# Kernel optimization log

Measured on AMD Instinct MI355X. Metric: run time of the kernel, lower is better.

Reference implementation:

```python
import jax, jax.numpy as jnp
import numpy as np

D_MODEL = 768
NUM_HEADS = 12
D_K = D_MODEL // NUM_HEADS
D_FF = 2048
LN_EPS = 1e-3  # Keras LayerNormalization default
B, S = 4, 2048


def layer_norm(x, gamma, beta):
    mu = jnp.mean(x, axis=-1, keepdims=True)
    var = jnp.var(x, axis=-1, keepdims=True)
    return (x - mu) * jax.lax.rsqrt(var + LN_EPS) * gamma + beta


def setup_inputs() -> dict:
    key = jax.random.key(0)
    ks = jax.random.split(key, 16)
    sd = 0.02
    inp = {
        "x": jax.random.normal(ks[0], (B, S, D_MODEL), dtype=jnp.float32),
        "src_mask": jnp.zeros((B, 1, 1, S), dtype=jnp.float32),
        "Wq": jax.random.normal(ks[1], (D_MODEL, D_MODEL), jnp.float32) * sd,
        "bq": jnp.zeros((D_MODEL,), jnp.float32),
        "Wk": jax.random.normal(ks[2], (D_MODEL, D_MODEL), jnp.float32) * sd,
        "bk": jnp.zeros((D_MODEL,), jnp.float32),
        "Wv": jax.random.normal(ks[3], (D_MODEL, D_MODEL), jnp.float32) * sd,
        "bv": jnp.zeros((D_MODEL,), jnp.float32),
        "Wo": jax.random.normal(ks[4], (D_MODEL, D_MODEL), jnp.float32) * sd,
        "bo": jnp.zeros((D_MODEL,), jnp.float32),
        "W1": jax.random.normal(ks[5], (D_MODEL, D_FF), jnp.float32) * sd,
        "b1": jnp.zeros((D_FF,), jnp.float32),
        "W2": jax.random.normal(ks[6], (D_FF, D_MODEL), jnp.float32) * sd,
        "b2": jnp.zeros((D_MODEL,), jnp.float32),
        "gamma1": jnp.ones((D_MODEL,), jnp.float32),
        "beta1": jnp.zeros((D_MODEL,), jnp.float32),
        "gamma2": jnp.ones((D_MODEL,), jnp.float32),
        "beta2": jnp.zeros((D_MODEL,), jnp.float32),
    }
    return inp


def encoder_layer(x, src_mask, Wq, bq, Wk, bk, Wv, bv, Wo, bo, W1, b1, W2, b2,
                  gamma1, beta1, gamma2, beta2):
    b, s, _ = x.shape
    def heads(t):  # [B,S,D] -> [B,H,S,Dk]
        return t.reshape(b, s, NUM_HEADS, D_K).transpose(0, 2, 1, 3)
    Q = heads(x @ Wq + bq)
    K = heads(x @ Wk + bk)
    V = heads(x @ Wv + bv)
    scores = jnp.einsum("bhqd,bhkd->bhqk", Q, K) / jnp.sqrt(jnp.float32(D_K))
    scores = scores + src_mask * (-1e9)
    probs = jax.nn.softmax(scores, axis=-1)
    attn = jnp.einsum("bhqk,bhkd->bhqd", probs, V)
    attn = attn.transpose(0, 2, 1, 3).reshape(b, s, D_MODEL)
    attn_out = attn @ Wo + bo
    # dropout is identity at inference
    x1 = layer_norm(x + attn_out, gamma1, beta1)
    ff = jax.nn.relu(x1 @ W1 + b1) @ W2 + b2
    return layer_norm(x1 + ff, gamma2, beta2)


def reference(x, src_mask, Wq, bq, Wk, bk, Wv, bv, Wo, bo, W1, b1, W2, b2,
              gamma1, beta1, gamma2, beta2):
    return encoder_layer(x, src_mask, Wq, bq, Wk, bk, Wv, bv, Wo, bo,
                         W1, b1, W2, b2, gamma1, beta1, gamma2, beta2)
```

## Files before the change

kernel.cpp:

```cpp
#include <hip/hip_runtime.h>


typedef unsigned short u16;
typedef __bf16 bf16x8 __attribute__((ext_vector_type(8)));
typedef __bf16 bf16x4 __attribute__((ext_vector_type(4)));
typedef unsigned short u16x8 __attribute__((ext_vector_type(8)));
typedef float f32x4 __attribute__((ext_vector_type(4)));

#define D_MODEL 768
#define D_FF    2048
#define NH      12
#define DK      64
#define S_LEN   2048
#define M_TOK   8192

#define QSCALE   0.18033688011112042f
#define MSCALE  -1.4426950408889634e9f

__device__ __forceinline__ float bf2f(u16 v) {
    union { unsigned u; float f; } c; c.u = ((unsigned)v) << 16; return c.f;
}
__device__ __forceinline__ void st_bf(u16* p, float v) { *(__bf16*)p = (__bf16)v; }

__device__ __forceinline__ void gload_lds16(const void* g, void* l) {
    __builtin_amdgcn_global_load_lds(
        (const __attribute__((address_space(1))) void*)g,
        (__attribute__((address_space(3))) void*)l, 16, 0, 0);
}

__global__ __launch_bounds__(256)
void prep_k(const float* __restrict__ x, const float* __restrict__ Wq,
            const float* __restrict__ Wk, const float* __restrict__ Wv,
            const float* __restrict__ Wo, const float* __restrict__ W1,
            const float* __restrict__ W2, u16* __restrict__ xb,
            u16* __restrict__ WqkvT, u16* __restrict__ WoT,
            u16* __restrict__ W1T, u16* __restrict__ W2T) {
    __shared__ float t[32][33];
    const int id = blockIdx.x, tid = threadIdx.x;
    if (id >= 5376) {
        const int i = ((id - 5376) * 256 + tid) * 4;
        const float4 v = *(const float4*)(x + i);
        __bf16 o[4] = {(__bf16)v.x, (__bf16)v.y, (__bf16)v.z, (__bf16)v.w};
        *(bf16x4*)(xb + i) = *(bf16x4*)o;
        return;
    }
    const float* in; u16* out; int R, C, bx, by;
    if (id < 2304) {
        const int z = id / 576, r = id % 576;
        in = z == 0 ? Wq : (z == 1 ? Wk : (z == 2 ? Wv : Wo));
        out = z == 3 ? WoT : WqkvT + z * 768 * 768;
        R = 768; C = 768; bx = (r % 24) * 32; by = (r / 24) * 32;
    } else if (id < 3840) {
        const int r = id - 2304;
        in = W1; out = W1T; R = 768; C = 2048;
        bx = (r % 64) * 32; by = (r / 64) * 32;
    } else {
        const int r = id - 3840;
        in = W2; out = W2T; R = 2048; C = 768;
        bx = (r % 24) * 32; by = (r / 24) * 32;
    }
    const int tx = tid & 31, ty = tid >> 5;
#pragma unroll
    for (int i = 0; i < 32; i += 8)
        t[ty + i][tx] = in[(size_t)(by + ty + i) * C + bx + tx];
    __syncthreads();
#pragma unroll
    for (int i = 0; i < 32; i += 8)
        st_bf(&out[(size_t)(bx + ty + i) * R + by + tx], t[tx][ty + i]);
}

__global__ __launch_bounds__(256, 2)
void qkv_gemm_k(const u16* __restrict__ A, const u16* __restrict__ Bt,
                const float* __restrict__ bq, const float* __restrict__ bk,
                const float* __restrict__ bv, u16* __restrict__ Qb,
                u16* __restrict__ Kb, u16* __restrict__ Vt) {
    __shared__ __align__(16) u16 As[2][128 * 32];
    __shared__ __align__(16) u16 Bs[2][128 * 32];
    const int tid = threadIdx.x;
    const int lane = tid & 63, w = tid >> 6;
    const int r16 = lane & 15, qd = lane >> 4;
    const int m0 = blockIdx.x * 128, n0 = blockIdx.y * 128;
    const int wm = (w & 1) << 6, wn = (w >> 1) << 6;
    const int K = D_MODEL;

    f32x4 acc[4][4] = {};

    const u16* aP[2]; const u16* bP[2]; int f8[2];
#pragma unroll
    for (int it = 0; it < 2; ++it) {
        const int f = it * 256 + tid;
        const int row = f >> 2, kc = (f & 3) << 3;
        aP[it] = A  + (size_t)(m0 + row) * K + kc;
        bP[it] = Bt + (size_t)(n0 + row) * K + kc;
        f8[it] = f * 8;
    }

    for (int k0 = 0; k0 < K; k0 += 64) {
#pragma unroll
        for (int p = 0; p < 2; ++p)
#pragma unroll
            for (int it = 0; it < 2; ++it) {
                gload_lds16(aP[it] + k0 + p * 32, &As[p][f8[it]]);
                gload_lds16(bP[it] + k0 + p * 32, &Bs[p][f8[it]]);
            }
        __syncthreads();
#pragma unroll
        for (int p = 0; p < 2; ++p) {
            bf16x8 af[4], bfr[4];
#pragma unroll
            for (int i = 0; i < 4; ++i) {
                af[i]  = *(const bf16x8*)&As[p][(wm + i * 16 + r16) * 32 + qd * 8];
                bfr[i] = *(const bf16x8*)&Bs[p][(wn + i * 16 + r16) * 32 + qd * 8];
            }
#pragma unroll
            for (int i = 0; i < 4; ++i)
#pragma unroll
                for (int j = 0; j < 4; ++j)
                    acc[i][j] = __builtin_amdgcn_mfma_f32_16x16x32_bf16(af[i], bfr[j], acc[i][j], 0, 0, 0);
        }
        __syncthreads();
    }

    const int sel = n0 < 768 ? 0 : (n0 < 1536 ? 1 : 2);
    const float* bias = sel == 0 ? bq : (sel == 1 ? bk : bv);
    const float scale = sel == 0 ? QSCALE : 1.0f;
    const int nbase = n0 - sel * 768;

#pragma unroll
    for (int j = 0; j < 4; ++j) {
        const int ncol = nbase + wn + j * 16 + r16;
        const float bvv = bias[ncol];
#pragma unroll
        for (int i = 0; i < 4; ++i) {
            if (sel == 2) {
                const int h = ncol >> 6, d = ncol & 63;
                const int mb = m0 + wm + i * 16 + qd * 4;
                const int bb = mb >> 11, npb = mb & 2047;
                __bf16 pk[4];
#pragma unroll
                for (int rr = 0; rr < 4; ++rr) pk[rr] = (__bf16)(acc[i][j][rr] + bvv);
                *(bf16x4*)&Vt[(((size_t)(bb * NH + h)) * DK + d) * S_LEN + npb] = *(bf16x4*)pk;
            } else {
#pragma unroll
                for (int rr = 0; rr < 4; ++rr) {
                    const int m = m0 + wm + i * 16 + qd * 4 + rr;
                    const float v = (acc[i][j][rr] + bvv) * scale;
                    if (sel == 0) st_bf(&Qb[(size_t)m * D_MODEL + ncol], v);
                    else          st_bf(&Kb[(size_t)m * D_MODEL + ncol], v);
                }
            }
        }
    }
}

__global__ __launch_bounds__(256, 2)
void gemm_bt_k(const u16* __restrict__ A, const u16* __restrict__ Bt,
               const float* __restrict__ bias, u16* __restrict__ Cout,
               int M, int N, int K, int mode) {
    __shared__ __align__(16) u16 As[2][128 * 32];
    __shared__ __align__(16) u16 Bs[2][128 * 32];
    const int tid = threadIdx.x;
    const int lane = tid & 63, w = tid >> 6;
    const int r16 = lane & 15, qd = lane >> 4;
    const int m0 = blockIdx.x * 128, n0 = blockIdx.y * 128;
    const int wm = (w & 1) << 6, wn = (w >> 1) << 6;

    f32x4 acc[4][4] = {};

    const u16* aP[2]; const u16* bP[2]; int f8[2];
#pragma unroll
    for (int it = 0; it < 2; ++it) {
        const int f = it * 256 + tid;
        const int row = f >> 2, kc = (f & 3) << 3;
        aP[it] = A  + (size_t)(m0 + row) * K + kc;
        bP[it] = Bt + (size_t)(n0 + row) * K + kc;
        f8[it] = f * 8;
    }

    for (int k0 = 0; k0 < K; k0 += 64) {
#pragma unroll
        for (int p = 0; p < 2; ++p)
#pragma unroll
            for (int it = 0; it < 2; ++it) {
                gload_lds16(aP[it] + k0 + p * 32, &As[p][f8[it]]);
                gload_lds16(bP[it] + k0 + p * 32, &Bs[p][f8[it]]);
            }
        __syncthreads();
#pragma unroll
        for (int p = 0; p < 2; ++p) {
            bf16x8 af[4], bfr[4];
#pragma unroll
            for (int i = 0; i < 4; ++i) {
                af[i]  = *(const bf16x8*)&As[p][(wm + i * 16 + r16) * 32 + qd * 8];
                bfr[i] = *(const bf16x8*)&Bs[p][(wn + i * 16 + r16) * 32 + qd * 8];
            }
#pragma unroll
            for (int i = 0; i < 4; ++i)
#pragma unroll
                for (int j = 0; j < 4; ++j)
                    acc[i][j] = __builtin_amdgcn_mfma_f32_16x16x32_bf16(af[i], bfr[j], acc[i][j], 0, 0, 0);
        }
        __syncthreads();
    }

#pragma unroll
    for (int j = 0; j < 4; ++j) {
        const int n = n0 + wn + j * 16 + r16;
        const float bv = bias ? bias[n] : 0.0f;
#pragma unroll
        for (int i = 0; i < 4; ++i) {
#pragma unroll
            for (int rr = 0; rr < 4; ++rr) {
                const int m = m0 + wm + i * 16 + qd * 4 + rr;
                float v = acc[i][j][rr] + bv;
                if (mode == 2) v = fmaxf(v, 0.0f);
                st_bf(&Cout[(size_t)m * N + n], v);
            }
        }
    }
}

__global__ __launch_bounds__(256, 3)
void gemm_bt64_k(const u16* __restrict__ A, const u16* __restrict__ Bt,
                 const float* __restrict__ bias, u16* __restrict__ Cout,
                 int M, int N, int K, int mode) {
    __shared__ __align__(16) u16 As[2][64 * 32];
    __shared__ __align__(16) u16 Bs[2][128 * 32];
    const int tid = threadIdx.x;
    const int lane = tid & 63, w = tid >> 6;
    const int r16 = lane & 15, qd = lane >> 4;
    const int m0 = blockIdx.x * 64, n0 = blockIdx.y * 128;
    const int wm = (w & 1) << 5, wn = (w >> 1) << 6;

    f32x4 acc[2][4] = {};

    const int arow = tid >> 2, akc = (tid & 3) << 3;
    const u16* aP = A + (size_t)(m0 + arow) * K + akc;
    const u16* bP[2]; int f8[2];
#pragma unroll
    for (int it = 0; it < 2; ++it) {
        const int f = it * 256 + tid;
        const int row = f >> 2, kc = (f & 3) << 3;
        bP[it] = Bt + (size_t)(n0 + row) * K + kc;
        f8[it] = f * 8;
    }

    for (int k0 = 0; k0 < K; k0 += 64) {
#pragma unroll
        for (int p = 0; p < 2; ++p) {
            gload_lds16(aP + k0 + p * 32, &As[p][tid * 8]);
#pragma unroll
            for (int it = 0; it < 2; ++it)
                gload_lds16(bP[it] + k0 + p * 32, &Bs[p][f8[it]]);
        }
        __syncthreads();
#pragma unroll
        for (int p = 0; p < 2; ++p) {
            bf16x8 af[2], bfr[4];
#pragma unroll
            for (int i = 0; i < 2; ++i)
                af[i] = *(const bf16x8*)&As[p][(wm + i * 16 + r16) * 32 + qd * 8];
#pragma unroll
            for (int j = 0; j < 4; ++j)
                bfr[j] = *(const bf16x8*)&Bs[p][(wn + j * 16 + r16) * 32 + qd * 8];
#pragma unroll
            for (int i = 0; i < 2; ++i)
#pragma unroll
                for (int j = 0; j < 4; ++j)
                    acc[i][j] = __builtin_amdgcn_mfma_f32_16x16x32_bf16(af[i], bfr[j], acc[i][j], 0, 0, 0);
        }
        __syncthreads();
    }

#pragma unroll
    for (int j = 0; j < 4; ++j) {
        const int n = n0 + wn + j * 16 + r16;
        const float bv = bias ? bias[n] : 0.0f;
#pragma unroll
        for (int i = 0; i < 2; ++i) {
#pragma unroll
            for (int rr = 0; rr < 4; ++rr) {
                const int m = m0 + wm + i * 16 + qd * 4 + rr;
                float v = acc[i][j][rr] + bv;
                if (mode == 2) v = fmaxf(v, 0.0f);
                st_bf(&Cout[(size_t)m * N + n], v);
            }
        }
    }
}

#define TS 72

__global__ __launch_bounds__(256, 3)
void attn_k(const u16* __restrict__ Qg, const u16* __restrict__ Kg,
            const u16* __restrict__ Vtg, const float* __restrict__ maskg,
            u16* __restrict__ Og) {
    const int tid = threadIdx.x, lane = tid & 63, w = tid >> 6;
    const int r16 = lane & 15, qd = lane >> 4;
    const int q0 = blockIdx.x * 128;
    const int h = blockIdx.y, b = blockIdx.z;

    __shared__ __align__(16) u16 Ks[64 * TS];
    __shared__ __align__(16) u16 Vts[64 * TS];
    __shared__ __align__(16) u16 Ps[128 * TS];

    bf16x8 qa[2][2];
#pragma unroll
    for (int mt = 0; mt < 2; ++mt)
#pragma unroll
        for (int ks = 0; ks < 2; ++ks)
            qa[mt][ks] = *(const bf16x8*)(Qg +
                ((size_t)((b * S_LEN + q0 + w * 32 + mt * 16 + r16) * NH + h)) * DK +
                ks * 32 + qd * 8);

    const int srow = tid >> 3, sc = (tid & 7) << 3;
    u16x8 kreg[2], vreg[2];
#pragma unroll
    for (int it = 0; it < 2; ++it) {
        const int row = srow + it * 32;
        kreg[it] = *(const u16x8*)(Kg + ((size_t)((b * S_LEN + row) * NH + h)) * DK + sc);
        vreg[it] = *(const u16x8*)(Vtg + (((size_t)(b * NH + h)) * DK + row) * S_LEN + sc);
    }

    float l_i[2] = {0.0f, 0.0f};
    f32x4 Oacc[2][4] = {};

    for (int kt = 0; kt < S_LEN / 64; ++kt) {
        const int ks0 = kt * 64;

#pragma unroll
        for (int it = 0; it < 2; ++it) {
            const int row = srow + it * 32;
            *(u16x8*)&Ks[row * TS + sc]  = kreg[it];
            *(u16x8*)&Vts[row * TS + sc] = vreg[it];
        }

        float4 mrow[4];
#pragma unroll
        for (int nt = 0; nt < 4; ++nt) {
            const float4 mm = ((const float4*)(maskg + (size_t)b * S_LEN + ks0))[nt * 4 + qd];
            mrow[nt].x = mm.x * MSCALE; mrow[nt].y = mm.y * MSCALE;
            mrow[nt].z = mm.z * MSCALE; mrow[nt].w = mm.w * MSCALE;
        }
        __syncthreads();

        if (kt + 1 < S_LEN / 64) {
            const int ns0 = ks0 + 64;
#pragma unroll
            for (int it = 0; it < 2; ++it) {
                const int row = srow + it * 32;
                kreg[it] = *(const u16x8*)(Kg + ((size_t)((b * S_LEN + ns0 + row) * NH + h)) * DK + sc);
                vreg[it] = *(const u16x8*)(Vtg + (((size_t)(b * NH + h)) * DK + row) * S_LEN + ns0 + sc);
            }
        }

        f32x4 sa[2][4];
#pragma unroll
        for (int mt = 0; mt < 2; ++mt)
#pragma unroll
            for (int nt = 0; nt < 4; ++nt) {
                sa[mt][nt][0] = mrow[nt].x; sa[mt][nt][1] = mrow[nt].y;
                sa[mt][nt][2] = mrow[nt].z; sa[mt][nt][3] = mrow[nt].w;
            }
#pragma unroll
        for (int ks = 0; ks < 2; ++ks) {
            bf16x8 kb[4];
#pragma unroll
            for (int nt = 0; nt < 4; ++nt)
                kb[nt] = *(const bf16x8*)&Ks[(nt * 16 + r16) * TS + ks * 32 + qd * 8];
#pragma unroll
            for (int mt = 0; mt < 2; ++mt)
#pragma unroll
                for (int nt = 0; nt < 4; ++nt)
                    sa[mt][nt] = __builtin_amdgcn_mfma_f32_16x16x32_bf16(kb[nt], qa[mt][ks], sa[mt][nt], 0, 0, 0);
        }

#pragma unroll
        for (int mt = 0; mt < 2; ++mt) {
            float rsum = 0.0f;
#pragma unroll
            for (int nt = 0; nt < 4; ++nt) {
                sa[mt][nt][0] = __builtin_amdgcn_exp2f(sa[mt][nt][0]);
                sa[mt][nt][1] = __builtin_amdgcn_exp2f(sa[mt][nt][1]);
                sa[mt][nt][2] = __builtin_amdgcn_exp2f(sa[mt][nt][2]);
                sa[mt][nt][3] = __builtin_amdgcn_exp2f(sa[mt][nt][3]);
                rsum += sa[mt][nt][0] + sa[mt][nt][1] + sa[mt][nt][2] + sa[mt][nt][3];
            }
            rsum += __shfl_xor(rsum, 16);
            rsum += __shfl_xor(rsum, 32);
            l_i[mt] += rsum;
        }

#pragma unroll
        for (int mt = 0; mt < 2; ++mt)
#pragma unroll
            for (int nt = 0; nt < 4; ++nt) {
                __bf16 pk[4];
#pragma unroll
                for (int rr = 0; rr < 4; ++rr) pk[rr] = (__bf16)sa[mt][nt][rr];
                *(bf16x4*)&Ps[(w * 32 + mt * 16 + r16) * TS + nt * 16 + qd * 4] = *(bf16x4*)pk;
            }

#pragma unroll
        for (int ks = 0; ks < 2; ++ks) {
            bf16x8 pa[2], vb[4];
#pragma unroll
            for (int mt = 0; mt < 2; ++mt)
                pa[mt] = *(const bf16x8*)&Ps[(w * 32 + mt * 16 + r16) * TS + ks * 32 + qd * 8];
#pragma unroll
            for (int vt = 0; vt < 4; ++vt)
                vb[vt] = *(const bf16x8*)&Vts[(vt * 16 + r16) * TS + ks * 32 + qd * 8];
#pragma unroll
            for (int mt = 0; mt < 2; ++mt)
#pragma unroll
                for (int vt = 0; vt < 4; ++vt)
                    Oacc[mt][vt] = __builtin_amdgcn_mfma_f32_16x16x32_bf16(pa[mt], vb[vt], Oacc[mt][vt], 0, 0, 0);
        }
        __syncthreads();
    }

#pragma unroll
    for (int mt = 0; mt < 2; ++mt) {
        const float linv = 1.0f / l_i[mt];
#pragma unroll
        for (int rr = 0; rr < 4; ++rr) {
            const float lr = __shfl(linv, qd * 4 + rr);
            const int qrow = q0 + w * 32 + mt * 16 + qd * 4 + rr;
#pragma unroll
            for (int vt = 0; vt < 4; ++vt)
                st_bf(&Og[((size_t)((b * S_LEN + qrow) * NH + h)) * DK + vt * 16 + r16],
                      Oacc[mt][vt][rr] * lr);
        }
    }
}

__global__ __launch_bounds__(256, 4)
void resln_k(const u16* __restrict__ xb, const u16* __restrict__ yb,
             const float* __restrict__ gamma, const float* __restrict__ beta,
             u16* __restrict__ outb, float* __restrict__ outf) {
    const int row = blockIdx.x, tid = threadIdx.x;
    const int lane = tid & 63, w = tid >> 6;
    __shared__ float redS[4], redS2[4];
    const size_t base = (size_t)row * D_MODEL;
    float h[3], s = 0.0f, s2 = 0.0f;
#pragma unroll
    for (int i = 0; i < 3; ++i) {
        const int c = i * 256 + tid;
        const float v = bf2f(xb[base + c]) + bf2f(yb[base + c]);
        h[i] = v; s += v; s2 += v * v;
    }
#pragma unroll
    for (int off = 32; off >= 1; off >>= 1) { s += __shfl_xor(s, off); s2 += __shfl_xor(s2, off); }
    if (lane == 0) { redS[w] = s; redS2[w] = s2; }
    __syncthreads();
    s  = redS[0] + redS[1] + redS[2] + redS[3];
    s2 = redS2[0] + redS2[1] + redS2[2] + redS2[3];
    const float mu  = s * (1.0f / D_MODEL);
    const float var = s2 * (1.0f / D_MODEL) - mu * mu;
    const float rstd = rsqrtf(var + 1e-3f);
#pragma unroll
    for (int i = 0; i < 3; ++i) {
        const int c = i * 256 + tid;
        const float o = (h[i] - mu) * rstd * gamma[c] + beta[c];
        if (outb) st_bf(&outb[base + c], o);
        if (outf) outf[base + c] = o;
    }
}

extern "C" void kernel_launch(void* const* d_in, const int* in_sizes, int n_in,
                              void* d_out, int out_size, void* d_ws, size_t ws_size,
                              hipStream_t stream) {
    (void)in_sizes; (void)n_in; (void)out_size; (void)ws_size;
    const float* x    = (const float*)d_in[0];
    const float* mask = (const float*)d_in[1];
    const float* Wq = (const float*)d_in[2];  const float* bq  = (const float*)d_in[3];
    const float* Wk = (const float*)d_in[4];  const float* bk  = (const float*)d_in[5];
    const float* Wv = (const float*)d_in[6];  const float* bv  = (const float*)d_in[7];
    const float* Wo = (const float*)d_in[8];  const float* bo  = (const float*)d_in[9];
    const float* W1 = (const float*)d_in[10]; const float* b1  = (const float*)d_in[11];
    const float* W2 = (const float*)d_in[12]; const float* b2  = (const float*)d_in[13];
    const float* g1 = (const float*)d_in[14]; const float* be1 = (const float*)d_in[15];
    const float* g2 = (const float*)d_in[16]; const float* be2 = (const float*)d_in[17];

    char* ws = (char*)d_ws;
    u16* xb     = (u16*)(ws + 0);
    u16* WqkvT  = (u16*)(ws + 12582912);
    u16* WoT    = (u16*)(ws + 16121856);
    u16* W1T    = (u16*)(ws + 17301504);
    u16* W2T    = (u16*)(ws + 20447232);
    u16* Qb     = (u16*)(ws + 23592960);
    u16* Kb     = (u16*)(ws + 36175872);
    u16* Vtg    = (u16*)(ws + 48758784);
    u16* Ab     = (u16*)(ws + 61341696);
    u16* Yb     = (u16*)(ws + 73924608);
    u16* X1b    = (u16*)(ws + 86507520);
    u16* H1b    = (u16*)(ws + 23592960);
    u16* Y2b    = (u16*)(ws + 73924608);

    const dim3 blk(256);

    prep_k<<<dim3(11520), blk, 0, stream>>>(x, Wq, Wk, Wv, Wo, W1, W2,
                                            xb, WqkvT, WoT, W1T, W2T);

    qkv_gemm_k<<<dim3(64, 18), blk, 0, stream>>>(xb, WqkvT, bq, bk, bv, Qb, Kb, Vtg);

    attn_k<<<dim3(16, NH, 4), blk, 0, stream>>>(Qb, Kb, Vtg, mask, Ab);

    gemm_bt64_k<<<dim3(128, 6), blk, 0, stream>>>(Ab, WoT, bo, Yb, M_TOK, D_MODEL, D_MODEL, 1);

    resln_k<<<dim3(M_TOK), blk, 0, stream>>>(xb, Yb, g1, be1, X1b, nullptr);

    gemm_bt_k<<<dim3(64, 16), blk, 0, stream>>>(X1b, W1T, b1, H1b, M_TOK, D_FF, D_MODEL, 2);

    gemm_bt64_k<<<dim3(128, 6), blk, 0, stream>>>(H1b, W2T, b2, Y2b, M_TOK, D_MODEL, D_FF, 1);

    resln_k<<<dim3(M_TOK), blk, 0, stream>>>(X1b, Y2b, g2, be2, nullptr, (float*)d_out);
}
```

Measured before the change: 353.1 us.

## Stream K from global, double-buffer V in LDS, drop per-tile barrier

The attention kernel no longer stages K in shared memory. Each wave reads its K fragments straight from global memory. V is now double-buffered in LDS, which lets the loop drop the trailing __syncthreads and run with one barrier per key tile. The change also wraps the MFMA blocks in s_setprio and raises launch bounds to 4 blocks per CU, aiming to cut barrier stalls and LDS pressure and to raise occupancy. In exchange, every wave fetches the same K tile from global memory, which adds L1/L2 traffic and exposes that load latency, and the tighter register budget could cause spills.

```diff
diff --git a/kernel.cpp b/kernel.cpp
--- a/kernel.cpp
+++ b/kernel.cpp
@@ -291,7 +291,7 @@
 
 #define TS 72
 
-__global__ __launch_bounds__(256, 3)
+__global__ __launch_bounds__(256, 4)
 void attn_k(const u16* __restrict__ Qg, const u16* __restrict__ Kg,
             const u16* __restrict__ Vtg, const float* __restrict__ maskg,
             u16* __restrict__ Og) {
@@ -300,8 +300,7 @@
     const int q0 = blockIdx.x * 128;
     const int h = blockIdx.y, b = blockIdx.z;
 
-    __shared__ __align__(16) u16 Ks[64 * TS];
-    __shared__ __align__(16) u16 Vts[64 * TS];
+    __shared__ __align__(16) u16 Vts[2][64 * TS];
     __shared__ __align__(16) u16 Ps[128 * TS];
 
     bf16x8 qa[2][2];
@@ -314,65 +313,61 @@
                 ks * 32 + qd * 8);
 
     const int srow = tid >> 3, sc = (tid & 7) << 3;
-    u16x8 kreg[2], vreg[2];
-#pragma unroll
-    for (int it = 0; it < 2; ++it) {
-        const int row = srow + it * 32;
-        kreg[it] = *(const u16x8*)(Kg + ((size_t)((b * S_LEN + row) * NH + h)) * DK + sc);
-        vreg[it] = *(const u16x8*)(Vtg + (((size_t)(b * NH + h)) * DK + row) * S_LEN + sc);
-    }
+    const u16* vsrc = Vtg + (((size_t)(b * NH + h)) * DK) * S_LEN;
+    u16x8 vreg[2];
+#pragma unroll
+    for (int it = 0; it < 2; ++it)
+        vreg[it] = *(const u16x8*)(vsrc + (size_t)(srow + it * 32) * S_LEN + sc);
+
+    const u16* kbase = Kg + ((size_t)b * S_LEN * NH + h) * DK;
+    const int kcol = qd * 8;
 
     float l_i[2] = {0.0f, 0.0f};
     f32x4 Oacc[2][4] = {};
 
     for (int kt = 0; kt < S_LEN / 64; ++kt) {
+        u16* vts = Vts[kt & 1];
         const int ks0 = kt * 64;
 
 #pragma unroll
-        for (int it = 0; it < 2; ++it) {
-            const int row = srow + it * 32;
-            *(u16x8*)&Ks[row * TS + sc]  = kreg[it];
-            *(u16x8*)&Vts[row * TS + sc] = vreg[it];
-        }
-
-        float4 mrow[4];
+        for (int it = 0; it < 2; ++it)
+            *(u16x8*)&vts[(srow + it * 32) * TS + sc] = vreg[it];
+        __syncthreads();
+
+        if (kt + 1 < S_LEN / 64) {
+#pragma unroll
+            for (int it = 0; it < 2; ++it)
+                vreg[it] = *(const u16x8*)(vsrc + (size_t)(srow + it * 32) * S_LEN +
+                                           ks0 + 64 + sc);
+        }
+
+        f32x4 sa[2][4];
 #pragma unroll
         for (int nt = 0; nt < 4; ++nt) {
             const float4 mm = ((const float4*)(maskg + (size_t)b * S_LEN + ks0))[nt * 4 + qd];
-            mrow[nt].x = mm.x * MSCALE; mrow[nt].y = mm.y * MSCALE;
-            mrow[nt].z = mm.z * MSCALE; mrow[nt].w = mm.w * MSCALE;
-        }
-        __syncthreads();
-
-        if (kt + 1 < S_LEN / 64) {
-            const int ns0 = ks0 + 64;
-#pragma unroll
-            for (int it = 0; it < 2; ++it) {
-                const int row = srow + it * 32;
-                kreg[it] = *(const u16x8*)(Kg + ((size_t)((b * S_LEN + ns0 + row) * NH + h)) * DK + sc);
-                vreg[it] = *(const u16x8*)(Vtg + (((size_t)(b * NH + h)) * DK + row) * S_LEN + ns0 + sc);
-            }
-        }
-
-        f32x4 sa[2][4];
-#pragma unroll
-        for (int mt = 0; mt < 2; ++mt)
-#pragma unroll
-            for (int nt = 0; nt < 4; ++nt) {
-                sa[mt][nt][0] = mrow[nt].x; sa[mt][nt][1] = mrow[nt].y;
-                sa[mt][nt][2] = mrow[nt].z; sa[mt][nt][3] = mrow[nt].w;
-            }
+            const float m0v = mm.x * MSCALE, m1v = mm.y * MSCALE,
+                        m2v = mm.z * MSCALE, m3v = mm.w * MSCALE;
+#pragma unroll
+            for (int mt = 0; mt < 2; ++mt) {
+                sa[mt][nt][0] = m0v; sa[mt][nt][1] = m1v;
+                sa[mt][nt][2] = m2v; sa[mt][nt][3] = m3v;
+            }
+        }
+
 #pragma unroll
         for (int ks = 0; ks < 2; ++ks) {
             bf16x8 kb[4];
 #pragma unroll
             for (int nt = 0; nt < 4; ++nt)
-                kb[nt] = *(const bf16x8*)&Ks[(nt * 16 + r16) * TS + ks * 32 + qd * 8];
+                kb[nt] = *(const bf16x8*)(kbase +
+                    (size_t)(ks0 + nt * 16 + r16) * (NH * DK) + ks * 32 + kcol);
+            __builtin_amdgcn_s_setprio(1);
 #pragma unroll
             for (int mt = 0; mt < 2; ++mt)
 #pragma unroll
                 for (int nt = 0; nt < 4; ++nt)
                     sa[mt][nt] = __builtin_amdgcn_mfma_f32_16x16x32_bf16(kb[nt], qa[mt][ks], sa[mt][nt], 0, 0, 0);
+            __builtin_amdgcn_s_setprio(0);
         }
 
 #pragma unroll
@@ -409,14 +404,15 @@
                 pa[mt] = *(const bf16x8*)&Ps[(w * 32 + mt * 16 + r16) * TS + ks * 32 + qd * 8];
 #pragma unroll
             for (int vt = 0; vt < 4; ++vt)
-                vb[vt] = *(const bf16x8*)&Vts[(vt * 16 + r16) * TS + ks * 32 + qd * 8];
+                vb[vt] = *(const bf16x8*)&vts[(vt * 16 + r16) * TS + ks * 32 + qd * 8];
+            __builtin_amdgcn_s_setprio(1);
 #pragma unroll
             for (int mt = 0; mt < 2; ++mt)
 #pragma unroll
                 for (int vt = 0; vt < 4; ++vt)
                     Oacc[mt][vt] = __builtin_amdgcn_mfma_f32_16x16x32_bf16(pa[mt], vb[vt], Oacc[mt][vt], 0, 0, 0);
-        }
-        __syncthreads();
+            __builtin_amdgcn_s_setprio(0);
+        }
     }
 
 #pragma unroll
```

After: 406.4 us. 15.1% more time.
